# Performance work log

Hardware: AMD Instinct MI355X
Metric: run time of the kernel (lower is better)

The kernel has to match this reference:

```python
import jax, jax.numpy as jnp
from jax import lax
import numpy as np

D = 128      # embedding_dim == GRU input_size == hidden_size
B, S, L = 256, 32, 32  # users, slates per user, slate length


def setup_inputs() -> dict:
    key = jax.random.key(0)
    ks = jax.random.split(key, 8)
    sc = 1.0 / np.sqrt(D)  # PyTorch GRU/Linear init scale
    return {
        "item_embs": jax.random.normal(ks[0], (B, S, L, D), jnp.float32),
        "user_embs": jax.random.normal(ks[1], (B, S, D), jnp.float32),
        "W_ih": jax.random.normal(ks[2], (3 * D, D), jnp.float32) * sc,
        "W_hh": jax.random.normal(ks[3], (3 * D, D), jnp.float32) * sc,
        "b_ih": jax.random.normal(ks[4], (3 * D,), jnp.float32) * sc,
        "b_hh": jax.random.normal(ks[5], (3 * D,), jnp.float32) * sc,
        "W_out": jax.random.normal(ks[6], (1, D), jnp.float32) * sc,
        "b_out": jax.random.normal(ks[7], (1,), jnp.float32) * sc,
    }


def reference(item_embs, user_embs, W_ih, W_hh, b_ih, b_hh, W_out, b_out):
    b, s, l, d = item_embs.shape
    x = item_embs.reshape(b * s, l, d)          # [N, L, D]
    h0 = user_embs.reshape(b * s, d)            # [N, D] initial hidden per slate

    # Precompute input-side gate projections for all timesteps (one big GEMM).
    gx = jnp.einsum('nld,gd->nlg', x, W_ih) + b_ih  # [N, L, 3D], PyTorch gate order r,z,n

    def step(h, gx_t):
        gh = h @ W_hh.T + b_hh                   # [N, 3D]
        xr, xz, xn = jnp.split(gx_t, 3, axis=-1)
        hr, hz, hn = jnp.split(gh, 3, axis=-1)
        r = jax.nn.sigmoid(xr + hr)
        z = jax.nn.sigmoid(xz + hz)
        n = jnp.tanh(xn + r * hn)
        h_new = (1.0 - z) * n + z * h
        return h_new, h_new

    _, hs = lax.scan(step, h0, jnp.swapaxes(gx, 0, 1))  # hs: [L, N, D]
    rnn_out = jnp.swapaxes(hs, 0, 1)             # [N, L, D]
    out = rnn_out @ W_out.T + b_out              # [N, L, 1]
    return out.reshape(b, s, l)
```

## Files before the change

### kernel.cpp

```cpp
#include <hip/hip_runtime.h>
#include <math.h>

#define DD   128
#define LL   32
#define MS   32
#define NT   512
#define NSEQ 8192
#define XHP  264
#define OLP  36

typedef short bf16x8 __attribute__((ext_vector_type(8)));
typedef float f32x4  __attribute__((ext_vector_type(4)));

__device__ __forceinline__ unsigned short f2bf(float f) {
    unsigned u = __float_as_uint(f);
    u += 0x7fffu + ((u >> 16) & 1u);
    return (unsigned short)(u >> 16);
}

__device__ __forceinline__ void pack8(float4 a, float4 b, unsigned short* dst) {
    union { unsigned short s[8]; bf16x8 v; } pk;
    pk.s[0] = f2bf(a.x); pk.s[1] = f2bf(a.y); pk.s[2] = f2bf(a.z); pk.s[3] = f2bf(a.w);
    pk.s[4] = f2bf(b.x); pk.s[5] = f2bf(b.y); pk.s[6] = f2bf(b.z); pk.s[7] = f2bf(b.w);
    *(bf16x8*)dst = pk.v;
}

__global__ void prep_weights(const float* __restrict__ Wih,
                             const float* __restrict__ Whh,
                             unsigned short* __restrict__ Wfrag) {
    int idx = blockIdx.x * blockDim.x + threadIdx.x;
    int j    = idx & 7;
    int lane = (idx >> 3) & 63;
    int kk   = (idx >> 9) & 7;
    int ct   = idx >> 12;
    int n = lane & 15, q = lane >> 4;
    float v = 0.f;
    if (ct < 16) {
        int g = ct * 16 + n;
        int k = kk * 32 + q * 8 + j;
        v = (k < 128) ? Wih[g * 128 + k] : Whh[g * 128 + (k - 128)];
    } else if (ct < 24) {
        if (kk < 4) {
            int g = 256 + (ct - 16) * 16 + n;
            int k = kk * 32 + q * 8 + j;
            v = Wih[g * 128 + k];
        }
    } else {
        if (kk >= 4) {
            int g = 256 + (ct - 24) * 16 + n;
            int k = kk * 32 + q * 8 + j - 128;
            v = Whh[g * 128 + k];
        }
    }
    Wfrag[idx] = f2bf(v);
}

__global__ __launch_bounds__(NT, 2) void gru_mfma(
    const float* __restrict__ x,
    const float* __restrict__ h0,
    const unsigned short* __restrict__ Wfrag,
    const float* __restrict__ b_ih,
    const float* __restrict__ b_hh,
    const float* __restrict__ w_out,
    const float* __restrict__ b_out,
    float* __restrict__ out)
{
    __shared__ __align__(16) unsigned short xh[2][MS][XHP];
    __shared__ __align__(16) unsigned short wofl[4 * 64 * 8];
    __shared__ __align__(16) float outl[MS][OLP];

    const int tid  = threadIdx.x;
    const int n0   = blockIdx.x * MS;
    const int wv   = tid >> 6;
    const int lane = tid & 63;
    const int ln   = lane & 15;
    const int q    = lane >> 4;
    const int gn   = tid >> 4;
    const int gd8  = (tid & 15) * 8;
    const int d    = wv * 16 + ln;

    const float br  = b_ih[d]        + b_hh[d];
    const float bz  = b_ih[DD + d]   + b_hh[DD + d];
    const float bin = b_ih[2*DD + d];
    const float bhn = b_hh[2*DD + d];
    const float bo  = b_out[0];

    bf16x8 wrz0[8], wrz1[8], wxn[4], whn[4];
    {
        const bf16x8* W = (const bf16x8*)Wfrag;
        #pragma unroll
        for (int kk = 0; kk < 8; ++kk) {
            wrz0[kk] = W[((wv    ) * 8 + kk) * 64 + lane];
            wrz1[kk] = W[((wv + 8) * 8 + kk) * 64 + lane];
        }
        #pragma unroll
        for (int kk = 0; kk < 4; ++kk) {
            wxn[kk] = W[((wv + 16) * 8 + kk    ) * 64 + lane];
            whn[kk] = W[((wv + 24) * 8 + kk + 4) * 64 + lane];
        }
    }

    #pragma unroll
    for (int e = 0; e < 4; ++e) {
        int idx = tid * 4 + e;
        int j   = idx & 7;
        int l2  = (idx >> 3) & 63;
        int kk  = idx >> 9;
        int n2 = l2 & 15, q2 = l2 >> 4;
        wofl[idx] = (n2 == 0) ? f2bf(w_out[kk * 32 + q2 * 8 + j])
                              : (unsigned short)0;
    }

    float hprev[8];
    #pragma unroll
    for (int tl = 0; tl < 2; ++tl)
        #pragma unroll
        for (int i = 0; i < 4; ++i)
            hprev[tl*4+i] = h0[(size_t)(n0 + tl*16 + q*4 + i) * DD + d];

    {
        const float* hb = h0 + (size_t)(n0 + gn) * DD + gd8;
        pack8(*(const float4*)hb, *(const float4*)(hb + 4), &xh[0][gn][DD + gd8]);
    }
    const float* xbase = x + ((size_t)(n0 + gn) * LL) * DD + gd8;
    pack8(*(const float4*)xbase, *(const float4*)(xbase + 4), &xh[0][gn][gd8]);
    float4 xa0 = *(const float4*)(xbase + 1 * DD);
    float4 xa1 = *(const float4*)(xbase + 1 * DD + 4);
    float4 xb0 = *(const float4*)(xbase + 2 * DD);
    float4 xb1 = *(const float4*)(xbase + 2 * DD + 4);
    __syncthreads();

#define GRU_STEP(PAR, XR0, XR1, TCUR, TREFILL)                                 \
    {                                                                          \
                       \
        pack8(XR0, XR1, &xh[(PAR) ^ 1][gn][gd8]);                              \
        XR0 = *(const float4*)(xbase + (size_t)(TREFILL) * DD);                \
        XR1 = *(const float4*)(xbase + (size_t)(TREFILL) * DD + 4);            \
                 \
        f32x4 c0[2], c1[2], c2[2], c3[2];                                      \
        _Pragma("unroll")                                                      \
        for (int tl = 0; tl < 2; ++tl) {                                       \
            c0[tl] = (f32x4){0.f,0.f,0.f,0.f}; c1[tl] = c0[tl];                \
            c2[tl] = c0[tl]; c3[tl] = c0[tl];                                  \
        }                                                                      \
        const unsigned short* xr0 = &xh[PAR][ln][0];                           \
        const unsigned short* xr1 = &xh[PAR][16 + ln][0];                      \
        _Pragma("unroll")                                                      \
        for (int kk = 0; kk < 8; ++kk) {                                       \
            bf16x8 a0 = *(const bf16x8*)(xr0 + kk*32 + q*8);                   \
            bf16x8 a1 = *(const bf16x8*)(xr1 + kk*32 + q*8);                   \
            c0[0] = __builtin_amdgcn_mfma_f32_16x16x32_bf16(a0, wrz0[kk], c0[0],0,0,0); \
            c0[1] = __builtin_amdgcn_mfma_f32_16x16x32_bf16(a1, wrz0[kk], c0[1],0,0,0); \
            c1[0] = __builtin_amdgcn_mfma_f32_16x16x32_bf16(a0, wrz1[kk], c1[0],0,0,0); \
            c1[1] = __builtin_amdgcn_mfma_f32_16x16x32_bf16(a1, wrz1[kk], c1[1],0,0,0); \
            if (kk < 4) {                                                      \
                c2[0] = __builtin_amdgcn_mfma_f32_16x16x32_bf16(a0, wxn[kk], c2[0],0,0,0); \
                c2[1] = __builtin_amdgcn_mfma_f32_16x16x32_bf16(a1, wxn[kk], c2[1],0,0,0); \
            } else {                                                           \
                c3[0] = __builtin_amdgcn_mfma_f32_16x16x32_bf16(a0, whn[kk-4], c3[0],0,0,0); \
                c3[1] = __builtin_amdgcn_mfma_f32_16x16x32_bf16(a1, whn[kk-4], c3[1],0,0,0); \
            }                                                                  \
        }                                                                      \
             \
        if (wv < 2 && (TCUR) > 0) {                                            \
            f32x4 c4 = {0.f,0.f,0.f,0.f};                                      \
            const unsigned short* xr = (wv == 0) ? xr0 : xr1;                  \
            _Pragma("unroll")                                                  \
            for (int kk = 0; kk < 4; ++kk) {                                   \
                bf16x8 a = *(const bf16x8*)(xr + (kk+4)*32 + q*8);             \
                bf16x8 b = *(const bf16x8*)&wofl[(kk*64 + lane)*8];            \
                c4 = __builtin_amdgcn_mfma_f32_16x16x32_bf16(a, b, c4,0,0,0);  \
            }                                                                  \
            if (ln == 0) {                                                     \
                _Pragma("unroll")                                              \
                for (int i = 0; i < 4; ++i)                                    \
                    outl[wv*16 + q*4 + i][(TCUR)-1] = c4[i] + bo;              \
            }                                                                  \
        }                                                                      \
                    \
        _Pragma("unroll")                                                      \
        for (int tl = 0; tl < 2; ++tl) {                                       \
            _Pragma("unroll")                                                  \
            for (int i = 0; i < 4; ++i) {                                      \
                const float rr = 1.f / (1.f + __expf(-(c0[tl][i] + br)));      \
                const float zz = 1.f / (1.f + __expf(-(c1[tl][i] + bz)));      \
                float aa = c2[tl][i] + bin + rr * (c3[tl][i] + bhn);           \
                aa = fminf(fmaxf(aa, -20.f), 20.f);                            \
                const float ee = __expf(-2.f * aa);                            \
                const float th = (1.f - ee) / (1.f + ee);                      \
                const float hh = (1.f - zz) * th + zz * hprev[tl*4+i];         \
                hprev[tl*4+i] = hh;                                            \
                xh[(PAR) ^ 1][tl*16 + q*4 + i][DD + d] = f2bf(hh);             \
            }                                                                  \
        }                                                                      \
        __syncthreads();                                                       \
    }

    for (int t = 0; t < LL; t += 2) {
        const int r0 = (t + 3 < LL) ? t + 3 : LL - 1;
        const int r1 = (t + 4 < LL) ? t + 4 : LL - 1;
        GRU_STEP(0, xa0, xa1, t,     r0)
        GRU_STEP(1, xb0, xb1, t + 1, r1)
    }
#undef GRU_STEP

    if (wv < 2) {
        f32x4 c4 = {0.f,0.f,0.f,0.f};
        const unsigned short* xr = &xh[0][wv*16 + ln][0];
        #pragma unroll
        for (int kk = 0; kk < 4; ++kk) {
            bf16x8 a = *(const bf16x8*)(xr + (kk+4)*32 + q*8);
            bf16x8 b = *(const bf16x8*)&wofl[(kk*64 + lane)*8];
            c4 = __builtin_amdgcn_mfma_f32_16x16x32_bf16(a, b, c4,0,0,0);
        }
        if (ln == 0) {
            #pragma unroll
            for (int i = 0; i < 4; ++i)
                outl[wv*16 + q*4 + i][LL-1] = c4[i] + bo;
        }
    }
    __syncthreads();

    if (tid < 256) {
        const int row = tid >> 3;
        const int t4  = (tid & 7) * 4;
        float4 v = *(const float4*)&outl[row][t4];
        *(float4*)(out + (size_t)(n0 + row) * LL + t4) = v;
    }
}

extern "C" void kernel_launch(void* const* d_in, const int* in_sizes, int n_in,
                              void* d_out, int out_size, void* d_ws, size_t ws_size,
                              hipStream_t stream) {
    const float* item  = (const float*)d_in[0];
    const float* user  = (const float*)d_in[1];
    const float* W_ih  = (const float*)d_in[2];
    const float* W_hh  = (const float*)d_in[3];
    const float* b_ih  = (const float*)d_in[4];
    const float* b_hh  = (const float*)d_in[5];
    const float* W_out = (const float*)d_in[6];
    const float* b_out = (const float*)d_in[7];
    float* out = (float*)d_out;

    unsigned short* Wfrag = (unsigned short*)d_ws;

    prep_weights<<<512, 256, 0, stream>>>(W_ih, W_hh, Wfrag);
    gru_mfma<<<NSEQ / MS, NT, 0, stream>>>(item, user, Wfrag,
                                           b_ih, b_hh, W_out, b_out, out);
}
```

Measured before the change: 245.3 us.

## Halve sequences per block to 16 and raise occupancy, use fast rcp and packed bf16 cvt

Each block now handles 16 sequences instead of 32, doubling the grid and halving per-thread accumulators and hidden-state registers, with launch bounds raised to 4 blocks per CU to improve latency hiding of the serial recurrence. Gate nonlinearities use a hardware reciprocal instead of division, and bf16 packing uses a packed convert builtin when available. The trade-off is that each weight fragment loaded into registers is reused across half as many sequences, only half the threads do x staging, and the tighter register budget risks spills.

New measurement: 405.5 us. +65.3%, slower.

```diff
diff --git a/kernel.cpp b/kernel.cpp
--- a/kernel.cpp
+++ b/kernel.cpp
@@ -3,7 +3,7 @@
 
 #define DD   128
 #define LL   32
-#define MS   32
+#define MS   16
 #define NT   512
 #define NSEQ 8192
 #define XHP  264
@@ -18,11 +18,28 @@
     return (unsigned short)(u >> 16);
 }
 
+#if __has_builtin(__builtin_amdgcn_cvt_pk_bf16_f32)
+typedef __bf16 bf16x2_t __attribute__((ext_vector_type(2)));
+__device__ __forceinline__ unsigned pack2(float a, float b) {
+    union { bf16x2_t v; unsigned u; } c;
+    c.v = __builtin_amdgcn_cvt_pk_bf16_f32(a, b);
+    return c.u;
+}
+#else
+__device__ __forceinline__ unsigned pack2(float a, float b) {
+    return (unsigned)f2bf(a) | ((unsigned)f2bf(b) << 16);
+}
+#endif
+
 __device__ __forceinline__ void pack8(float4 a, float4 b, unsigned short* dst) {
-    union { unsigned short s[8]; bf16x8 v; } pk;
-    pk.s[0] = f2bf(a.x); pk.s[1] = f2bf(a.y); pk.s[2] = f2bf(a.z); pk.s[3] = f2bf(a.w);
-    pk.s[4] = f2bf(b.x); pk.s[5] = f2bf(b.y); pk.s[6] = f2bf(b.z); pk.s[7] = f2bf(b.w);
+    union { unsigned u[4]; bf16x8 v; } pk;
+    pk.u[0] = pack2(a.x, a.y); pk.u[1] = pack2(a.z, a.w);
+    pk.u[2] = pack2(b.x, b.y); pk.u[3] = pack2(b.z, b.w);
     *(bf16x8*)dst = pk.v;
+}
+
+__device__ __forceinline__ float fast_rcp(float x) {
+    return __builtin_amdgcn_rcpf(x);
 }
 
 __global__ void prep_weights(const float* __restrict__ Wih,
@@ -55,7 +72,7 @@
     Wfrag[idx] = f2bf(v);
 }
 
-__global__ __launch_bounds__(NT, 2) void gru_mfma(
+__global__ __launch_bounds__(NT, 4) void gru_mfma(
     const float* __restrict__ x,
     const float* __restrict__ h0,
     const unsigned short* __restrict__ Wfrag,
@@ -75,7 +92,7 @@
     const int lane = tid & 63;
     const int ln   = lane & 15;
     const int q    = lane >> 4;
-    const int gn   = tid >> 4;
+    const int gn   = (tid >> 4) & 15;
     const int gd8  = (tid & 15) * 8;
     const int d    = wv * 16 + ln;
 
@@ -111,87 +128,70 @@
                               : (unsigned short)0;
     }
 
-    float hprev[8];
+    float hprev[4];
     #pragma unroll
-    for (int tl = 0; tl < 2; ++tl)
-        #pragma unroll
-        for (int i = 0; i < 4; ++i)
-            hprev[tl*4+i] = h0[(size_t)(n0 + tl*16 + q*4 + i) * DD + d];
-
-    {
+    for (int i = 0; i < 4; ++i)
+        hprev[i] = h0[(size_t)(n0 + q*4 + i) * DD + d];
+
+    const float* xbase = x + ((size_t)(n0 + gn) * LL) * DD + gd8;
+    float4 xa0, xa1, xb0, xb1;
+    if (tid < 256) {
         const float* hb = h0 + (size_t)(n0 + gn) * DD + gd8;
         pack8(*(const float4*)hb, *(const float4*)(hb + 4), &xh[0][gn][DD + gd8]);
-    }
-    const float* xbase = x + ((size_t)(n0 + gn) * LL) * DD + gd8;
-    pack8(*(const float4*)xbase, *(const float4*)(xbase + 4), &xh[0][gn][gd8]);
-    float4 xa0 = *(const float4*)(xbase + 1 * DD);
-    float4 xa1 = *(const float4*)(xbase + 1 * DD + 4);
-    float4 xb0 = *(const float4*)(xbase + 2 * DD);
-    float4 xb1 = *(const float4*)(xbase + 2 * DD + 4);
+        pack8(*(const float4*)xbase, *(const float4*)(xbase + 4), &xh[0][gn][gd8]);
+        xa0 = *(const float4*)(xbase + 1 * DD);
+        xa1 = *(const float4*)(xbase + 1 * DD + 4);
+        xb0 = *(const float4*)(xbase + 2 * DD);
+        xb1 = *(const float4*)(xbase + 2 * DD + 4);
+    }
     __syncthreads();
 
 #define GRU_STEP(PAR, XR0, XR1, TCUR, TREFILL)                                 \
     {                                                                          \
                        \
-        pack8(XR0, XR1, &xh[(PAR) ^ 1][gn][gd8]);                              \
-        XR0 = *(const float4*)(xbase + (size_t)(TREFILL) * DD);                \
-        XR1 = *(const float4*)(xbase + (size_t)(TREFILL) * DD + 4);            \
-                 \
-        f32x4 c0[2], c1[2], c2[2], c3[2];                                      \
-        _Pragma("unroll")                                                      \
-        for (int tl = 0; tl < 2; ++tl) {                                       \
-            c0[tl] = (f32x4){0.f,0.f,0.f,0.f}; c1[tl] = c0[tl];                \
-            c2[tl] = c0[tl]; c3[tl] = c0[tl];                                  \
-        }                                                                      \
+        if (tid < 256) {                                                       \
+            pack8(XR0, XR1, &xh[(PAR) ^ 1][gn][gd8]);                          \
+            XR0 = *(const float4*)(xbase + (size_t)(TREFILL) * DD);            \
+            XR1 = *(const float4*)(xbase + (size_t)(TREFILL) * DD + 4);        \
+        }                                                                      \
+                                   \
+        f32x4 c0 = {0.f,0.f,0.f,0.f}, c1 = c0, c2 = c0, c3 = c0;               \
         const unsigned short* xr0 = &xh[PAR][ln][0];                           \
-        const unsigned short* xr1 = &xh[PAR][16 + ln][0];                      \
         _Pragma("unroll")                                                      \
         for (int kk = 0; kk < 8; ++kk) {                                       \
             bf16x8 a0 = *(const bf16x8*)(xr0 + kk*32 + q*8);                   \
-            bf16x8 a1 = *(const bf16x8*)(xr1 + kk*32 + q*8);                   \
-            c0[0] = __builtin_amdgcn_mfma_f32_16x16x32_bf16(a0, wrz0[kk], c0[0],0,0,0); \
-            c0[1] = __builtin_amdgcn_mfma_f32_16x16x32_bf16(a1, wrz0[kk], c0[1],0,0,0); \
-            c1[0] = __builtin_amdgcn_mfma_f32_16x16x32_bf16(a0, wrz1[kk], c1[0],0,0,0); \
-            c1[1] = __builtin_amdgcn_mfma_f32_16x16x32_bf16(a1, wrz1[kk], c1[1],0,0,0); \
-            if (kk < 4) {                                                      \
-                c2[0] = __builtin_amdgcn_mfma_f32_16x16x32_bf16(a0, wxn[kk], c2[0],0,0,0); \
-                c2[1] = __builtin_amdgcn_mfma_f32_16x16x32_bf16(a1, wxn[kk], c2[1],0,0,0); \
-            } else {                                                           \
-                c3[0] = __builtin_amdgcn_mfma_f32_16x16x32_bf16(a0, whn[kk-4], c3[0],0,0,0); \
-                c3[1] = __builtin_amdgcn_mfma_f32_16x16x32_bf16(a1, whn[kk-4], c3[1],0,0,0); \
-            }                                                                  \
-        }                                                                      \
-             \
-        if (wv < 2 && (TCUR) > 0) {                                            \
+            c0 = __builtin_amdgcn_mfma_f32_16x16x32_bf16(a0, wrz0[kk], c0,0,0,0); \
+            c1 = __builtin_amdgcn_mfma_f32_16x16x32_bf16(a0, wrz1[kk], c1,0,0,0); \
+            if (kk < 4) c2 = __builtin_amdgcn_mfma_f32_16x16x32_bf16(a0, wxn[kk],   c2,0,0,0); \
+            else        c3 = __builtin_amdgcn_mfma_f32_16x16x32_bf16(a0, whn[kk-4], c3,0,0,0); \
+        }                                                                      \
+                         \
+        if (wv == 0 && (TCUR) > 0) {                                           \
             f32x4 c4 = {0.f,0.f,0.f,0.f};                                      \
-            const unsigned short* xr = (wv == 0) ? xr0 : xr1;                  \
             _Pragma("unroll")                                                  \
             for (int kk = 0; kk < 4; ++kk) {                                   \
-                bf16x8 a = *(const bf16x8*)(xr + (kk+4)*32 + q*8);             \
+                bf16x8 a = *(const bf16x8*)(xr0 + (kk+4)*32 + q*8);            \
                 bf16x8 b = *(const bf16x8*)&wofl[(kk*64 + lane)*8];            \
                 c4 = __builtin_amdgcn_mfma_f32_16x16x32_bf16(a, b, c4,0,0,0);  \
             }                                                                  \
             if (ln == 0) {                                                     \
                 _Pragma("unroll")                                              \
                 for (int i = 0; i < 4; ++i)                                    \
-                    outl[wv*16 + q*4 + i][(TCUR)-1] = c4[i] + bo;              \
+                    outl[q*4 + i][(TCUR)-1] = c4[i] + bo;                      \
             }                                                                  \
         }                                                                      \
-                    \
+                       \
         _Pragma("unroll")                                                      \
-        for (int tl = 0; tl < 2; ++tl) {                                       \
-            _Pragma("unroll")                                                  \
-            for (int i = 0; i < 4; ++i) {                                      \
-                const float rr = 1.f / (1.f + __expf(-(c0[tl][i] + br)));      \
-                const float zz = 1.f / (1.f + __expf(-(c1[tl][i] + bz)));      \
-                float aa = c2[tl][i] + bin + rr * (c3[tl][i] + bhn);           \
-                aa = fminf(fmaxf(aa, -20.f), 20.f);                            \
-                const float ee = __expf(-2.f * aa);                            \
-                const float th = (1.f - ee) / (1.f + ee);                      \
-                const float hh = (1.f - zz) * th + zz * hprev[tl*4+i];         \
-                hprev[tl*4+i] = hh;                                            \
-                xh[(PAR) ^ 1][tl*16 + q*4 + i][DD + d] = f2bf(hh);             \
-            }                                                                  \
+        for (int i = 0; i < 4; ++i) {                                          \
+            const float rr = fast_rcp(1.f + __expf(-(c0[i] + br)));            \
+            const float zz = fast_rcp(1.f + __expf(-(c1[i] + bz)));            \
+            float aa = c2[i] + bin + rr * (c3[i] + bhn);                       \
+            aa = fminf(fmaxf(aa, -20.f), 20.f);                                \
+            const float ee = __expf(-2.f * aa);                                \
+            const float th = (1.f - ee) * fast_rcp(1.f + ee);                  \
+            const float hh = th + zz * (hprev[i] - th);                        \
+            hprev[i] = hh;                                                     \
+            xh[(PAR) ^ 1][q*4 + i][DD + d] = f2bf(hh);                         \
         }                                                                      \
         __syncthreads();                                                       \
     }
@@ -204,9 +204,9 @@
     }
 #undef GRU_STEP
 
-    if (wv < 2) {
+    if (wv == 0) {
         f32x4 c4 = {0.f,0.f,0.f,0.f};
-        const unsigned short* xr = &xh[0][wv*16 + ln][0];
+        const unsigned short* xr = &xh[0][ln][0];
         #pragma unroll
         for (int kk = 0; kk < 4; ++kk) {
             bf16x8 a = *(const bf16x8*)(xr + (kk+4)*32 + q*8);
@@ -216,12 +216,12 @@
         if (ln == 0) {
             #pragma unroll
             for (int i = 0; i < 4; ++i)
-                outl[wv*16 + q*4 + i][LL-1] = c4[i] + bo;
+                outl[q*4 + i][LL-1] = c4[i] + bo;
         }
     }
     __syncthreads();
 
-    if (tid < 256) {
+    if (tid < 128) {
         const int row = tid >> 3;
         const int t4  = (tid & 7) * 4;
         float4 v = *(const float4*)&outl[row][t4];
```
